# Kernel tuning notes

Measured on AMD Instinct MI355X. Metric: run time of the kernel, lower is better.

## Reference

```python
import jax, jax.numpy as jnp
import numpy as np

N_NODES = 100000
N_EDGES = 3200000
D_COORD = 3
N_HIDDEN = 32
C_WEIGHT = 1.0


def setup_inputs() -> dict:
    key = jax.random.key(0)
    ks = jax.random.split(key, 12)
    x = jax.random.normal(ks[0], (N_NODES, D_COORD), dtype=jnp.float32)
    edge_index = jax.random.randint(ks[1], (2, N_EDGES), 0, N_NODES, dtype=jnp.int64)
    s = lambda fan_in: 1.0 / np.sqrt(fan_in)
    # phi_e: Linear(2->H, no bias), BN(H), ReLU, Linear(H->H), ReLU
    W1 = jax.random.uniform(ks[2], (2, N_HIDDEN), jnp.float32, -s(2), s(2))
    bn_gamma = jnp.ones((N_HIDDEN,), jnp.float32)
    bn_beta = jnp.zeros((N_HIDDEN,), jnp.float32)
    bn_mean = jnp.zeros((N_HIDDEN,), jnp.float32)
    bn_var = jnp.ones((N_HIDDEN,), jnp.float32)
    W2 = jax.random.uniform(ks[3], (N_HIDDEN, N_HIDDEN), jnp.float32, -s(N_HIDDEN), s(N_HIDDEN))
    b2 = jax.random.uniform(ks[4], (N_HIDDEN,), jnp.float32, -s(N_HIDDEN), s(N_HIDDEN))
    # phi_x: Linear(H->H), ReLU, Linear(H->1, no bias, xavier gain=0.001)
    W3 = jax.random.uniform(ks[5], (N_HIDDEN, N_HIDDEN), jnp.float32, -s(N_HIDDEN), s(N_HIDDEN))
    b3 = jax.random.uniform(ks[6], (N_HIDDEN,), jnp.float32, -s(N_HIDDEN), s(N_HIDDEN))
    xav = 0.001 * np.sqrt(6.0 / (N_HIDDEN + 1))
    W4 = jax.random.uniform(ks[7], (N_HIDDEN, 1), jnp.float32, -xav, xav)
    # phi_m: Linear(H->1), Sigmoid
    W5 = jax.random.uniform(ks[8], (N_HIDDEN, 1), jnp.float32, -s(N_HIDDEN), s(N_HIDDEN))
    b5 = jax.random.uniform(ks[9], (1,), jnp.float32, -s(N_HIDDEN), s(N_HIDDEN))
    return dict(x=x, edge_index=edge_index, W1=W1, bn_gamma=bn_gamma, bn_beta=bn_beta,
                bn_mean=bn_mean, bn_var=bn_var, W2=W2, b2=b2, W3=W3, b3=b3, W4=W4,
                W5=W5, b5=b5)


def _psi(t):
    # sign(t) * log(|t| + 1), the standard norm-squashing used in (Lorentz/E)GNN feats
    return jnp.sign(t) * jnp.log1p(jnp.abs(t))


def _forward(x, edge_index, W1, bn_gamma, bn_beta, bn_mean, bn_var, W2, b2, W3, b3, W4, W5, b5):
    i, j = edge_index[0], edge_index[1]
    xi = x[i]                                # [E, 3]
    xj = x[j]                                # [E, 3]
    x_diff = xi - xj                         # [E, 3]
    norms = _psi(jnp.sum(x_diff * x_diff, axis=1, keepdims=True))  # [E, 1]
    dots = _psi(jnp.sum(xi * xj, axis=1, keepdims=True))           # [E, 1]

    # message: phi_e (Linear no-bias -> BN eval -> ReLU -> Linear -> ReLU)
    m_ij = jnp.concatenate([norms, dots], axis=1)                   # [E, 2]
    h = m_ij @ W1                                                    # [E, H]
    h = (h - bn_mean) * (bn_gamma / jnp.sqrt(bn_var + 1e-5)) + bn_beta
    h = jax.nn.relu(h)
    h = jax.nn.relu(h @ W2 + b2)                                     # [E, H]
    w = jax.nn.sigmoid(h @ W5 + b5)                                  # [E, 1]
    m = h * w                                                        # [E, H]

    # x_model: phi_x then scatter-mean over destination node i
    phix = jax.nn.relu(m @ W3 + b3) @ W4                             # [E, 1]
    update_val = jnp.clip(x_diff * phix, -100.0, 100.0)              # [E, 3]
    sums = jax.ops.segment_sum(update_val, i, num_segments=x.shape[0])
    counts = jax.ops.segment_sum(jnp.ones((update_val.shape[0],), update_val.dtype),
                                 i, num_segments=x.shape[0])
    x_agg = sums / jnp.maximum(counts, 1.0)[:, None]
    x_tilde = x + x_agg * C_WEIGHT
    return x_tilde, m


def reference(x, edge_index, W1, bn_gamma, bn_beta, bn_mean, bn_var, W2, b2, W3, b3, W4, W5, b5):
    return _forward(x, edge_index, W1, bn_gamma, bn_beta, bn_mean, bn_var, W2, b2, W3, b3, W4, W5, b5)
```

## Files before the change

kernel.cpp:

```cpp
#include <hip/hip_runtime.h>
#include <math.h>

#define NN 100000
#define NE 3200000
#define H  32
#define NTILES (NE / 32)
#define EDGE_BLOCKS 3125
#define STRIDE (EDGE_BLOCKS * 4)
#define ITERS2 4

#define FXSCALE 131072.0f
#define FXBIAS  100.0f

typedef __attribute__((ext_vector_type(8)))  short bf8;
typedef __attribute__((ext_vector_type(16))) float f16x;
typedef __attribute__((ext_vector_type(4)))  unsigned int u32x4;

__device__ __forceinline__ short f2bf(float f) {
    union { float f; unsigned u; } v; v.f = f;
    unsigned r = (v.u + 0x7FFFu + ((v.u >> 16) & 1u)) >> 16;
    return (short)r;
}

__device__ __forceinline__ unsigned pk2(float lo, float hi) {
    unsigned r;
    asm("v_cvt_pk_bf16_f32 %0, %1, %2" : "=v"(r) : "v"(lo), "v"(hi));
    return r;
}

__device__ __forceinline__ bf8 mkfrag(unsigned a, unsigned b, unsigned c, unsigned d) {
    union { u32x4 u; bf8 s; } cv;
    cv.u = (u32x4){a, b, c, d};
    return cv.s;
}

__device__ __forceinline__ void packswap(const float* v, int half, bf8& B0, bf8& B1) {
    unsigned w0 = pk2(v[0],  v[1]),  w1 = pk2(v[2],  v[3]);
    unsigned w2 = pk2(v[4],  v[5]),  w3 = pk2(v[6],  v[7]);
    unsigned w4 = pk2(v[8],  v[9]),  w5 = pk2(v[10], v[11]);
    unsigned w6 = pk2(v[12], v[13]), w7 = pk2(v[14], v[15]);
    unsigned r0 = __shfl_xor(half ? w0 : w2, 32);
    unsigned r1 = __shfl_xor(half ? w1 : w3, 32);
    unsigned r2 = __shfl_xor(half ? w4 : w6, 32);
    unsigned r3 = __shfl_xor(half ? w5 : w7, 32);
    B0 = mkfrag(half ? r0 : w0, half ? r1 : w1, half ? w2 : r0, half ? w3 : r1);
    B1 = mkfrag(half ? r2 : w4, half ? r3 : w5, half ? w6 : r2, half ? w7 : r3);
}

__global__ __launch_bounds__(256) void edge_kernel(
    const float* __restrict__ x,
    const int* __restrict__ ei,
    const float* __restrict__ W1,
    const float* __restrict__ bn_g, const float* __restrict__ bn_b,
    const float* __restrict__ bn_m, const float* __restrict__ bn_v,
    const float* __restrict__ W2, const float* __restrict__ b2,
    const float* __restrict__ W3, const float* __restrict__ b3,
    const float* __restrict__ W4, const float* __restrict__ W5,
    const float* __restrict__ b5,
    float* __restrict__ m_out,
    unsigned long long* __restrict__ acc64)
{
    const int tid  = threadIdx.x;
    const int lane = tid & 63;
    const int n    = lane & 31;
    const int half = lane >> 5;

    bf8 W1a, W2a0, W2a1, W3a0, W3a1;
    #pragma unroll
    for (int q = 0; q < 8; q++) W1a[q] = 0;
    {
        float sc_n = bn_g[n] * rsqrtf(bn_v[n] + 1e-5f);
        float cf_n = bn_b[n] - bn_m[n] * sc_n;
        if (half == 0) {
            W1a[0] = f2bf(W1[n] * sc_n);
            W1a[1] = f2bf(W1[H + n] * sc_n);
            W1a[2] = f2bf(cf_n);
        }
    }
    #pragma unroll
    for (int j = 0; j < 8; j++) {
        int k0 = 8 * half + j;
        W2a0[j] = f2bf(W2[k0 * H + n]);
        W2a1[j] = f2bf(W2[(k0 + 16) * H + n]);
        W3a0[j] = f2bf(W3[k0 * H + n]);
        W3a1[j] = f2bf(W3[(k0 + 16) * H + n]);
    }
    const float b5v = b5[0];

    const int wid   = blockIdx.x * 4 + (tid >> 6);
    const int ebase = half ? NE : 0;

    int idxc[2], idxn[2];
    float xc[2][3], xn[2][3];
    #pragma unroll
    for (int p = 0; p < 2; p++) {
        idxc[p] = ei[ebase + (wid + p * STRIDE) * 32 + n];
        idxn[p] = ei[ebase + (wid + (2 + p) * STRIDE) * 32 + n];
    }
    #pragma unroll
    for (int p = 0; p < 2; p++) {
        const float* xp = x + 3 * idxc[p];
        xc[p][0] = xp[0]; xc[p][1] = xp[1]; xc[p][2] = xp[2];
    }

    #pragma unroll 1
    for (int it = 0; it < ITERS2; ++it) {
        const int itp = (it + 2 < ITERS2) ? (it + 2) : (ITERS2 - 1);
        int tile[2], idxp[2];
        #pragma unroll
        for (int p = 0; p < 2; p++) {
            tile[p] = wid + (2 * it + p) * STRIDE;
            idxp[p] = ei[ebase + (wid + (2 * itp + p) * STRIDE) * 32 + n];
        }
        #pragma unroll
        for (int p = 0; p < 2; p++) {
            const float* xp = x + 3 * idxn[p];
            xn[p][0] = xp[0]; xn[p][1] = xp[1]; xn[p][2] = xp[2];
        }

        float dx[2], dy[2], dz[2], nrm[2], dts[2];
        int iidx[2];
        #pragma unroll
        for (int p = 0; p < 2; p++) {
            float ox0 = __shfl_xor(xc[p][0], 32);
            float ox1 = __shfl_xor(xc[p][1], 32);
            float ox2 = __shfl_xor(xc[p][2], 32);
            int  oidx = __shfl_xor(idxc[p], 32);
            iidx[p] = half ? oidx : idxc[p];
            float xi0 = half ? ox0 : xc[p][0], xi1 = half ? ox1 : xc[p][1], xi2 = half ? ox2 : xc[p][2];
            float xj0 = half ? xc[p][0] : ox0, xj1 = half ? xc[p][1] : ox1, xj2 = half ? xc[p][2] : ox2;
            dx[p] = xi0 - xj0; dy[p] = xi1 - xj1; dz[p] = xi2 - xj2;
            float nsq = dx[p] * dx[p] + dy[p] * dy[p] + dz[p] * dz[p];
            float dot = xi0 * xj0 + xi1 * xj1 + xi2 * xj2;
            nrm[p] = __logf(1.f + nsq);
            dts[p] = copysignf(__logf(1.f + fabsf(dot)), dot);
        }

        f16x acc[2];
        #pragma unroll
        for (int p = 0; p < 2; p++) {
            unsigned nd = pk2(nrm[p], dts[p]);
            bf8 ndf = mkfrag(half ? 0u : nd, half ? 0u : 0x3F80u, 0u, 0u);
            f16x a;
            #pragma unroll
            for (int q = 0; q < 16; q++) a[q] = 0.f;
            acc[p] = __builtin_amdgcn_mfma_f32_32x32x16_bf16(W1a, ndf, a, 0, 0, 0);
        }

        float h2[2][16];
        #pragma unroll
        for (int p = 0; p < 2; p++) {
            float h1r[16];
            #pragma unroll
            for (int q = 0; q < 16; q++) h1r[q] = fmaxf(acc[p][q], 0.f);
            bf8 B0, B1;
            packswap(h1r, half, B0, B1);
            f16x a;
            #pragma unroll
            for (int g = 0; g < 4; g++) {
                float4 bb = ((const float4*)b2)[2 * g + half];
                a[4 * g + 0] = bb.x; a[4 * g + 1] = bb.y;
                a[4 * g + 2] = bb.z; a[4 * g + 3] = bb.w;
            }
            a = __builtin_amdgcn_mfma_f32_32x32x16_bf16(W2a0, B0, a, 0, 0, 0);
            a = __builtin_amdgcn_mfma_f32_32x32x16_bf16(W2a1, B1, a, 0, 0, 0);
            #pragma unroll
            for (int q = 0; q < 16; q++) h2[p][q] = fmaxf(a[q], 0.f);
        }

        float mm[2][16];
        #pragma unroll
        for (int p = 0; p < 2; p++) {
            float zp = 0.f;
            #pragma unroll
            for (int g = 0; g < 4; g++) {
                float4 wv = ((const float4*)W5)[2 * g + half];
                zp = fmaf(h2[p][4 * g + 0], wv.x, zp);
                zp = fmaf(h2[p][4 * g + 1], wv.y, zp);
                zp = fmaf(h2[p][4 * g + 2], wv.z, zp);
                zp = fmaf(h2[p][4 * g + 3], wv.w, zp);
            }
            float z = zp + __shfl_xor(zp, 32) + b5v;
            float wgt = 1.f / (1.f + __expf(-z));
            #pragma unroll
            for (int q = 0; q < 16; q++) mm[p][q] = h2[p][q] * wgt;
        }

        #pragma unroll
        for (int p = 0; p < 2; p++) {
            float* mb = m_out + (size_t)tile[p] * 1024 + n * 32 + 4 * half;
            #pragma unroll
            for (int g = 0; g < 4; g++) {
                *(float4*)(mb + 8 * g) =
                    make_float4(mm[p][4 * g], mm[p][4 * g + 1], mm[p][4 * g + 2], mm[p][4 * g + 3]);
            }
        }

        #pragma unroll
        for (int p = 0; p < 2; p++) {
            bf8 M0, M1;
            packswap(mm[p], half, M0, M1);
            f16x a;
            #pragma unroll
            for (int g = 0; g < 4; g++) {
                float4 bb = ((const float4*)b3)[2 * g + half];
                a[4 * g + 0] = bb.x; a[4 * g + 1] = bb.y;
                a[4 * g + 2] = bb.z; a[4 * g + 3] = bb.w;
            }
            a = __builtin_amdgcn_mfma_f32_32x32x16_bf16(W3a0, M0, a, 0, 0, 0);
            a = __builtin_amdgcn_mfma_f32_32x32x16_bf16(W3a1, M1, a, 0, 0, 0);
            float pp = 0.f;
            #pragma unroll
            for (int g = 0; g < 4; g++) {
                float4 wv = ((const float4*)W4)[2 * g + half];
                pp = fmaf(fmaxf(a[4 * g + 0], 0.f), wv.x, pp);
                pp = fmaf(fmaxf(a[4 * g + 1], 0.f), wv.y, pp);
                pp = fmaf(fmaxf(a[4 * g + 2], 0.f), wv.z, pp);
                pp = fmaf(fmaxf(a[4 * g + 3], 0.f), wv.w, pp);
            }
            float phix = pp + __shfl_xor(pp, 32);

            float ux = fminf(fmaxf(dx[p] * phix, -100.f), 100.f);
            float uy = fminf(fmaxf(dy[p] * phix, -100.f), 100.f);
            float uz = fminf(fmaxf(dz[p] * phix, -100.f), 100.f);

            unsigned qlo = __float2uint_rn(((half ? uz : ux) + FXBIAS) * FXSCALE);
            unsigned qhi = half ? __float2uint_rn((uy + FXBIAS) * FXSCALE) : 1u;
            unsigned long long payload = ((unsigned long long)qhi << 32) | (unsigned long long)qlo;
            atomicAdd(&acc64[2 * iidx[p] + half], payload);
        }

        #pragma unroll
        for (int p = 0; p < 2; p++) {
            idxc[p] = idxn[p]; idxn[p] = idxp[p];
            xc[p][0] = xn[p][0]; xc[p][1] = xn[p][1]; xc[p][2] = xn[p][2];
        }
    }
}

__global__ __launch_bounds__(256) void node_kernel(
    const float* __restrict__ x,
    const unsigned long long* __restrict__ acc64,
    float* __restrict__ out)
{
    int nn = blockIdx.x * blockDim.x + threadIdx.x;
    if (nn < NN) {
        unsigned long long a = acc64[2 * nn];
        unsigned long long b = acc64[2 * nn + 1];
        double cnt = (double)(unsigned)(a >> 32);
        const double inv17 = 1.0 / 131072.0;
        double bias = 100.0 * cnt;
        float sx = (float)((double)(unsigned)(a & 0xFFFFFFFFu) * inv17 - bias);
        float sy = (float)((double)(unsigned)(b >> 32)         * inv17 - bias);
        float sz = (float)((double)(unsigned)(b & 0xFFFFFFFFu) * inv17 - bias);
        float inv = 1.f / fmaxf((float)cnt, 1.f);
        out[3 * nn + 0] = x[3 * nn + 0] + sx * inv;
        out[3 * nn + 1] = x[3 * nn + 1] + sy * inv;
        out[3 * nn + 2] = x[3 * nn + 2] + sz * inv;
    }
}

extern "C" void kernel_launch(void* const* d_in, const int* in_sizes, int n_in,
                              void* d_out, int out_size, void* d_ws, size_t ws_size,
                              hipStream_t stream) {
    const float* x    = (const float*)d_in[0];
    const int*   ei   = (const int*)d_in[1];
    const float* W1   = (const float*)d_in[2];
    const float* bn_g = (const float*)d_in[3];
    const float* bn_b = (const float*)d_in[4];
    const float* bn_m = (const float*)d_in[5];
    const float* bn_v = (const float*)d_in[6];
    const float* W2   = (const float*)d_in[7];
    const float* b2   = (const float*)d_in[8];
    const float* W3   = (const float*)d_in[9];
    const float* b3   = (const float*)d_in[10];
    const float* W4   = (const float*)d_in[11];
    const float* W5   = (const float*)d_in[12];
    const float* b5   = (const float*)d_in[13];

    float* out    = (float*)d_out;
    float* m_out  = out + (size_t)3 * NN;
    unsigned long long* acc64 = (unsigned long long*)d_ws;

    hipMemsetAsync(d_ws, 0, (size_t)2 * NN * sizeof(unsigned long long), stream);

    edge_kernel<<<EDGE_BLOCKS, 256, 0, stream>>>(
        x, ei, W1, bn_g, bn_b, bn_m, bn_v, W2, b2, W3, b3, W4, W5, b5,
        m_out, acc64);

    node_kernel<<<(NN + 255) / 256, 256, 0, stream>>>(x, acc64, out);
}
```

Before: 605.9 us.

## Pack count and three coordinates into one 64-bit atomic with float fallback

Replaces the two 64-bit fixed-point atomics per edge with a single 64-bit atomic that packs a 7-bit count and three 19-bit fixed-point coordinates (bias 2, scale 1024). Edges with any component of magnitude 1.99 or more fall back to float atomics into a separate buffer. This halves atomic traffic to the accumulator and shrinks its footprint, at the cost of lower precision (about 1e-3 quantization) and possible field overflow if a node has more than 127 edges or many accumulated values.

```diff
diff --git a/kernel.cpp b/kernel.cpp
--- a/kernel.cpp
+++ b/kernel.cpp
@@ -9,8 +9,8 @@
 #define STRIDE (EDGE_BLOCKS * 4)
 #define ITERS2 4
 
-#define FXSCALE 131072.0f
-#define FXBIAS  100.0f
+#define FBIAS 2.0f
+#define FSCALE 1024.0f
 
 typedef __attribute__((ext_vector_type(8)))  short bf8;
 typedef __attribute__((ext_vector_type(16))) float f16x;
@@ -58,7 +58,8 @@
     const float* __restrict__ W4, const float* __restrict__ W5,
     const float* __restrict__ b5,
     float* __restrict__ m_out,
-    unsigned long long* __restrict__ acc64)
+    unsigned long long* __restrict__ acc64,
+    float* __restrict__ fb)
 {
     const int tid  = threadIdx.x;
     const int lane = tid & 63;
@@ -224,10 +225,22 @@
             float uy = fminf(fmaxf(dy[p] * phix, -100.f), 100.f);
             float uz = fminf(fmaxf(dz[p] * phix, -100.f), 100.f);
 
-            unsigned qlo = __float2uint_rn(((half ? uz : ux) + FXBIAS) * FXSCALE);
-            unsigned qhi = half ? __float2uint_rn((uy + FXBIAS) * FXSCALE) : 1u;
-            unsigned long long payload = ((unsigned long long)qhi << 32) | (unsigned long long)qlo;
-            atomicAdd(&acc64[2 * iidx[p] + half], payload);
+            if (half == 0) {
+                float amax = fmaxf(fmaxf(fabsf(ux), fabsf(uy)), fabsf(uz));
+                bool fast = amax < 1.99f;
+                unsigned qx = fast ? __float2uint_rn((ux + FBIAS) * FSCALE) : 2048u;
+                unsigned qy = fast ? __float2uint_rn((uy + FBIAS) * FSCALE) : 2048u;
+                unsigned qz = fast ? __float2uint_rn((uz + FBIAS) * FSCALE) : 2048u;
+                unsigned long long payload =
+                    (1ULL << 57) | ((unsigned long long)qx << 38) |
+                    ((unsigned long long)qy << 19) | (unsigned long long)qz;
+                atomicAdd(&acc64[iidx[p]], payload);
+                if (__builtin_expect(!fast, 0)) {
+                    atomicAdd(&fb[3 * iidx[p] + 0], ux);
+                    atomicAdd(&fb[3 * iidx[p] + 1], uy);
+                    atomicAdd(&fb[3 * iidx[p] + 2], uz);
+                }
+            }
         }
 
         #pragma unroll
@@ -241,18 +254,18 @@
 __global__ __launch_bounds__(256) void node_kernel(
     const float* __restrict__ x,
     const unsigned long long* __restrict__ acc64,
+    const float* __restrict__ fb,
     float* __restrict__ out)
 {
     int nn = blockIdx.x * blockDim.x + threadIdx.x;
     if (nn < NN) {
-        unsigned long long a = acc64[2 * nn];
-        unsigned long long b = acc64[2 * nn + 1];
-        double cnt = (double)(unsigned)(a >> 32);
-        const double inv17 = 1.0 / 131072.0;
-        double bias = 100.0 * cnt;
-        float sx = (float)((double)(unsigned)(a & 0xFFFFFFFFu) * inv17 - bias);
-        float sy = (float)((double)(unsigned)(b >> 32)         * inv17 - bias);
-        float sz = (float)((double)(unsigned)(b & 0xFFFFFFFFu) * inv17 - bias);
+        unsigned long long a = acc64[nn];
+        double cnt = (double)(unsigned)(a >> 57);
+        const double invs = 1.0 / 1024.0;
+        double bias = 2.0 * cnt;
+        float sx = (float)((double)((a >> 38) & 0x7FFFFu) * invs - bias) + fb[3 * nn + 0];
+        float sy = (float)((double)((a >> 19) & 0x7FFFFu) * invs - bias) + fb[3 * nn + 1];
+        float sz = (float)((double)( a        & 0x7FFFFu) * invs - bias) + fb[3 * nn + 2];
         float inv = 1.f / fmaxf((float)cnt, 1.f);
         out[3 * nn + 0] = x[3 * nn + 0] + sx * inv;
         out[3 * nn + 1] = x[3 * nn + 1] + sy * inv;
@@ -281,12 +294,13 @@
     float* out    = (float*)d_out;
     float* m_out  = out + (size_t)3 * NN;
     unsigned long long* acc64 = (unsigned long long*)d_ws;
-
-    hipMemsetAsync(d_ws, 0, (size_t)2 * NN * sizeof(unsigned long long), stream);
+    float* fb = (float*)(acc64 + NN);
+
+    hipMemsetAsync(d_ws, 0, (size_t)NN * 8 + (size_t)3 * NN * 4, stream);
 
     edge_kernel<<<EDGE_BLOCKS, 256, 0, stream>>>(
         x, ei, W1, bn_g, bn_b, bn_m, bn_v, W2, b2, W3, b3, W4, W5, b5,
-        m_out, acc64);
-
-    node_kernel<<<(NN + 255) / 256, 256, 0, stream>>>(x, acc64, out);
-}
+        m_out, acc64, fb);
+
+    node_kernel<<<(NN + 255) / 256, 256, 0, stream>>>(x, acc64, fb, out);
+}
```

New measurement: 600.0 us. No clear change (-1.0%).
